# Performance work log

Hardware: AMD Instinct MI355X
Metric: run time of the kernel (lower is better)

The kernel has to match this reference:

```python
import jax, jax.numpy as jnp
import numpy as np

N = 8192   # decoder nodes (batch*seq)
M = 8192   # encoder memory nodes
D = 512    # d_model (layer.size)
H = 8      # attention heads
DK = D // H
DFF = 2048 # feed-forward hidden
E = 262144 # edges per attention graph (avg in-degree 32)
EPS = 1e-6


def _ln(x, g, b):
    # LayerNorm over last dim (annotated-transformer style, eps=1e-6)
    mu = x.mean(-1, keepdims=True)
    var = ((x - mu) ** 2).mean(-1, keepdims=True)
    return (x - mu) * jax.lax.rsqrt(var + EPS) * g + b


def _heads(t):
    return t.reshape(-1, H, DK)


def _attend(q, k, v, src, dst, n_dst):
    # per-edge score = exp(clip(k_src . q_dst / sqrt(dk))), scatter-sum to dst
    score = jnp.einsum('ehd,ehd->eh', k[src], q[dst]) * np.float32(1.0 / np.sqrt(DK))
    score = jnp.exp(jnp.clip(score, -10.0, 10.0))
    wv = jax.ops.segment_sum(score[:, :, None] * v[src], dst, num_segments=n_dst)  # [n_dst,H,DK]
    z = jax.ops.segment_sum(score, dst, num_segments=n_dst)                         # [n_dst,H]
    return (wv / z[:, :, None]).reshape(n_dst, D)


def setup_inputs() -> dict:
    key = jax.random.key(0)
    ks = jax.random.split(key, 16)
    f = lambda k, shape, s: jax.random.normal(k, shape, dtype=jnp.float32) * np.float32(s)
    inp = {
        'x': f(ks[0], (N, D), 1.0),
        'mem': f(ks[1], (M, D), 1.0),
        'ln0_g': jnp.ones((D,), jnp.float32), 'ln0_b': jnp.zeros((D,), jnp.float32),
        'ln1_g': jnp.ones((D,), jnp.float32), 'ln1_b': jnp.zeros((D,), jnp.float32),
        'ln2_g': jnp.ones((D,), jnp.float32), 'ln2_b': jnp.zeros((D,), jnp.float32),
        'Wq': f(ks[2], (D, D), D ** -0.5), 'bq': jnp.zeros((D,), jnp.float32),
        'Wk': f(ks[3], (D, D), D ** -0.5), 'bk': jnp.zeros((D,), jnp.float32),
        'Wv': f(ks[4], (D, D), D ** -0.5), 'bv': jnp.zeros((D,), jnp.float32),
        'Wo': f(ks[5], (D, D), D ** -0.5), 'bo': jnp.zeros((D,), jnp.float32),
        'W1': f(ks[6], (D, DFF), D ** -0.5), 'b1': jnp.zeros((DFF,), jnp.float32),
        'W2': f(ks[7], (DFF, D), DFF ** -0.5), 'b2': jnp.zeros((D,), jnp.float32),
        'src_self': jax.random.randint(ks[8], (E,), 0, N),
        'dst_self': jax.random.randint(ks[9], (E,), 0, N),
        'src_cross': jax.random.randint(ks[10], (E,), 0, M),
        'dst_cross': jax.random.randint(ks[11], (E,), 0, N),
    }
    return inp


def reference(x, mem, ln0_g, ln0_b, ln1_g, ln1_b, ln2_g, ln2_b,
              Wq, bq, Wk, bk, Wv, bv, Wo, bo, W1, b1, W2, b2,
              src_self, dst_self, src_cross, dst_cross):
    # l=0: self-attention. pre_func('qkv',0): norm then qkv projections.
    h = _ln(x, ln0_g, ln0_b)
    q = _heads(h @ Wq + bq)
    k = _heads(h @ Wk + bk)
    v = _heads(h @ Wv + bv)
    # post_func(0): o = W_o(wv/z); x = x + dropout(o) (eval: identity)
    o = _attend(q, k, v, src_self, dst_self, N) @ Wo + bo
    x = x + o
    # l=1: cross-attention. pre_func('q',1): norm on decoder nodes;
    # pre_func('kv'): NO norm on memory nodes (norm_x = x branch).
    h = _ln(x, ln1_g, ln1_b)
    q = _heads(h @ Wq + bq)
    km = _heads(mem @ Wk + bk)
    vm = _heads(mem @ Wv + bv)
    o = _attend(q, km, vm, src_cross, dst_cross, N) @ Wo + bo
    x = x + o
    # post_func(1): feed-forward sublayer x + dropout(FF(LN(x)))
    h = _ln(x, ln2_g, ln2_b)
    x = x + (jax.nn.relu(h @ W1 + b1) @ W2 + b2)
    return x
```

## Files before the change

### kernel.cpp

```cpp
#include <hip/hip_runtime.h>
#include <cstdint>
#include <cstddef>

#define DEV __device__ __forceinline__

typedef __attribute__((ext_vector_type(4))) float f32x4;
typedef __attribute__((ext_vector_type(2))) float f32x2;
typedef __attribute__((ext_vector_type(4))) unsigned int u32x4;
typedef __attribute__((ext_vector_type(2))) unsigned int u32x2;
typedef unsigned short ushort_t;

constexpr int NN  = 8192;
constexpr int MMM = 8192;
constexpr int DD  = 512;
constexpr int DFF = 2048;

DEV unsigned short f2bf(float f) {
  unsigned int u = __builtin_bit_cast(unsigned int, f);
  u += 0x7fffu + ((u >> 16) & 1u);
  return (unsigned short)(u >> 16);
}
DEV float bflo(unsigned int u) { return __builtin_bit_cast(float, u << 16); }
DEV float bfhi(unsigned int u) { return __builtin_bit_cast(float, u & 0xffff0000u); }
DEV unsigned char f2fp8(float f) {
  int p = __builtin_amdgcn_cvt_pk_fp8_f32(f, f, 0, false);
  return (unsigned char)(p & 0xff);
}

DEV void gload_lds16(const void* g, void* l) {
  __builtin_amdgcn_global_load_lds((__attribute__((address_space(1))) void*)g,
                                   (__attribute__((address_space(3))) void*)l,
                                   16, 0, 0);
}

__global__ void transw_kernel(const float* __restrict__ in, ushort_t* __restrict__ out,
                              int R, int C) {
  __shared__ float t[32][33];
  const int x0 = blockIdx.x * 32, y0 = blockIdx.y * 32;
  const int tx = threadIdx.x, ty = threadIdx.y;
#pragma unroll
  for (int i = 0; i < 4; ++i)
    t[ty + i * 8][tx] = in[(long)(y0 + ty + i * 8) * C + x0 + tx];
  __syncthreads();
#pragma unroll
  for (int i = 0; i < 4; ++i)
    out[(long)(x0 + ty + i * 8) * R + y0 + tx] = f2bf(t[tx][ty + i * 8]);
}

struct TW4 {
  const float* in0; const float* in1; const float* in2; const float* in3;
  ushort_t* o0; ushort_t* o1; ushort_t* o2; ushort_t* o3;
};
__global__ void transw4_kernel(TW4 p) {
  const float* in; ushort_t* out;
  switch (blockIdx.z) {
    case 0:  in = p.in0; out = p.o0; break;
    case 1:  in = p.in1; out = p.o1; break;
    case 2:  in = p.in2; out = p.o2; break;
    default: in = p.in3; out = p.o3; break;
  }
  __shared__ float t[32][33];
  const int x0 = blockIdx.x * 32, y0 = blockIdx.y * 32;
  const int tx = threadIdx.x, ty = threadIdx.y;
#pragma unroll
  for (int i = 0; i < 4; ++i)
    t[ty + i * 8][tx] = in[(long)(y0 + ty + i * 8) * 512 + x0 + tx];
  __syncthreads();
#pragma unroll
  for (int i = 0; i < 4; ++i)
    out[(long)(x0 + ty + i * 8) * 512 + y0 + tx] = f2bf(t[tx][ty + i * 8]);
}

__global__ void tobf_kernel(const float* __restrict__ in, ushort_t* __restrict__ out, int n4) {
  int i = blockIdx.x * blockDim.x + threadIdx.x;
  if (i >= n4) return;
  f32x4 v = ((const f32x4*)in)[i];
  u32x2 o;
  o[0] = (unsigned)f2bf(v[0]) | ((unsigned)f2bf(v[1]) << 16);
  o[1] = (unsigned)f2bf(v[2]) | ((unsigned)f2bf(v[3]) << 16);
  ((u32x2*)out)[i] = o;
}

__global__ void biascat_kernel(const float* __restrict__ bq, const float* __restrict__ bk,
                               const float* __restrict__ bv, float* __restrict__ o) {
  const int i = blockIdx.x * blockDim.x + threadIdx.x;
  if (i >= 1536) return;
  o[i] = (i < 512) ? bq[i] : ((i < 1024) ? bk[i - 512] : bv[i - 1024]);
}

__global__ __launch_bounds__(256)
void ln_kernel(const float* __restrict__ x, const float* __restrict__ g,
               const float* __restrict__ b, ushort_t* __restrict__ out) {
  const int row  = blockIdx.x * 4 + (threadIdx.x >> 6);
  const int lane = threadIdx.x & 63;
  const float* xr = x + (long)row * DD + lane * 8;
  float v[8];
  *(f32x4*)&v[0] = *(const f32x4*)&xr[0];
  *(f32x4*)&v[4] = *(const f32x4*)&xr[4];
  float s = 0.f, sq = 0.f;
#pragma unroll
  for (int i = 0; i < 8; ++i) { s += v[i]; sq += v[i] * v[i]; }
#pragma unroll
  for (int o = 1; o < 64; o <<= 1) { s += __shfl_xor(s, o); sq += __shfl_xor(sq, o); }
  const float mu   = s * (1.f / 512.f);
  const float var  = sq * (1.f / 512.f) - mu * mu;
  const float rstd = rsqrtf(var + 1e-6f);
  const float* gp = g + lane * 8;
  const float* bp = b + lane * 8;
  u32x4 o8;
#pragma unroll
  for (int u = 0; u < 4; ++u) {
    unsigned int lo = f2bf((v[2 * u]     - mu) * rstd * gp[2 * u]     + bp[2 * u]);
    unsigned int hi = f2bf((v[2 * u + 1] - mu) * rstd * gp[2 * u + 1] + bp[2 * u + 1]);
    o8[u] = lo | (hi << 16);
  }
  *(u32x4*)(out + (long)row * DD + lane * 8) = o8;
}


template <int EPI>
__global__ __launch_bounds__(256, 2)
void gemm_kernel(const ushort_t* __restrict__ A, const ushort_t* __restrict__ Bt,
                 const float* __restrict__ bias, const float* res,
                 float* outF, ushort_t* outB, unsigned char* out8, int M, int N, int K) {
  __shared__ __align__(16) ushort_t sA[128 * 64];
  __shared__ __align__(16) ushort_t sB[128 * 64];
  const int tid  = threadIdx.x;
  const int lane = tid & 63;
  const int w    = tid >> 6;
  const int wr   = w >> 1, wc = w & 1;
  const long brow = (long)blockIdx.x * 128;
  const long bcol = (long)blockIdx.y * 128;
  const int r16 = lane & 15;
  const int cq  = lane >> 4;
  f32x4 acc[4][4] = {};

  for (int k0 = 0; k0 < K; k0 += 64) {
    __syncthreads();
#pragma unroll
    for (int i = 0; i < 4; ++i) {
      const int c   = i * 256 + tid;
      const int wb  = i * 256 + (tid & ~63);
      const int row = c >> 3;
      const int col = ((c & 7) ^ (row & 7)) << 3;
      gload_lds16(A  + (brow + row) * (long)K + k0 + col, &sA[(long)wb * 8]);
      gload_lds16(Bt + (bcol + row) * (long)K + k0 + col, &sB[(long)wb * 8]);
    }
    __syncthreads();
#pragma unroll
    for (int kkc = 0; kkc < 8; kkc += 4) {
      u32x4 af[4], bfr[4];
#pragma unroll
      for (int i = 0; i < 4; ++i) {
        const int row = wr * 64 + i * 16 + r16;
        af[i] = *(const u32x4*)&sA[row * 64 + (((kkc + cq) ^ (row & 7)) << 3)];
      }
#pragma unroll
      for (int j = 0; j < 4; ++j) {
        const int row = wc * 64 + j * 16 + r16;
        bfr[j] = *(const u32x4*)&sB[row * 64 + (((kkc + cq) ^ (row & 7)) << 3)];
      }
#pragma unroll
      for (int i = 0; i < 4; ++i)
#pragma unroll
        for (int j = 0; j < 4; ++j)
          asm("v_mfma_f32_16x16x32_bf16 %0, %1, %2, %0"
              : "+v"(acc[i][j]) : "v"(af[i]), "v"(bfr[j]));
    }
  }
  asm volatile("s_nop 7\n\ts_nop 7\n\ts_nop 7" ::);

  const long orow = brow + wr * 64;
  const long ocol = bcol + wc * 64;
#pragma unroll
  for (int j = 0; j < 4; ++j) {
    const long c  = ocol + j * 16 + r16;
    const float bv = bias[c];
#pragma unroll
    for (int i = 0; i < 4; ++i) {
      const long r0 = orow + i * 16 + ((lane >> 4) << 2);
#pragma unroll
      for (int r = 0; r < 4; ++r) {
        float v = acc[i][j][r] + bv;
        const long row = r0 + r;
        if (EPI == 0)      outB[row * (long)N + c] = f2bf(v);
        else if (EPI == 1) outB[row * (long)N + c] = f2bf(fmaxf(v, 0.f));
        else if (EPI == 2) outF[row * (long)N + c] = v + res[row * (long)N + c];
        else if (EPI == 3) out8[row * (long)N + c] = f2fp8(v);
        else {
          if (c < 512) outB[row * 512 + c] = f2bf(v);
          else         out8[row * 1024 + (c - 512)] = f2fp8(v);
        }
      }
    }
  }
}

template <int EPI>
__global__ __launch_bounds__(256, 4)
void gemm64b_kernel(const ushort_t* __restrict__ A, const ushort_t* __restrict__ Bt,
                    const float* __restrict__ bias, const float* res,
                    float* outF, ushort_t* outB, unsigned char* out8, int M, int N, int K) {
  __shared__ __align__(16) ushort_t sA[64 * 64];
  __shared__ __align__(16) ushort_t sB[64 * 64];
  const int tid  = threadIdx.x;
  const int lane = tid & 63;
  const int w    = tid >> 6;
  const int wr   = w >> 1, wc = w & 1;
  const long brow = (long)blockIdx.x * 64;
  const long bcol = (long)blockIdx.y * 64;
  const int r16 = lane & 15;
  const int cq  = lane >> 4;
  f32x4 acc[2][2] = {};

  for (int k0 = 0; k0 < K; k0 += 64) {
    __syncthreads();
#pragma unroll
    for (int i = 0; i < 2; ++i) {
      const int c   = i * 256 + tid;
      const int wb  = i * 256 + (tid & ~63);
      const int row = c >> 3;
      const int col = ((c & 7) ^ (row & 7)) << 3;
      gload_lds16(A  + (brow + row) * (long)K + k0 + col, &sA[(long)wb * 8]);
      gload_lds16(Bt + (bcol + row) * (long)K + k0 + col, &sB[(long)wb * 8]);
    }
    __syncthreads();
#pragma unroll
    for (int kkc = 0; kkc < 8; kkc += 4) {
      u32x4 af[2], bfr[2];
#pragma unroll
      for (int i = 0; i < 2; ++i) {
        const int row = wr * 32 + i * 16 + r16;
        af[i] = *(const u32x4*)&sA[row * 64 + (((kkc + cq) ^ (row & 7)) << 3)];
      }
#pragma unroll
      for (int j = 0; j < 2; ++j) {
        const int row = wc * 32 + j * 16 + r16;
        bfr[j] = *(const u32x4*)&sB[row * 64 + (((kkc + cq) ^ (row & 7)) << 3)];
      }
#pragma unroll
      for (int i = 0; i < 2; ++i)
#pragma unroll
        for (int j = 0; j < 2; ++j)
          asm("v_mfma_f32_16x16x32_bf16 %0, %1, %2, %0"
              : "+v"(acc[i][j]) : "v"(af[i]), "v"(bfr[j]));
    }
  }
  asm volatile("s_nop 7\n\ts_nop 7\n\ts_nop 7" ::);

  const long orow = brow + wr * 32;
  const long ocol = bcol + wc * 32;
#pragma unroll
  for (int j = 0; j < 2; ++j) {
    const long c  = ocol + j * 16 + r16;
    const float bv = bias[c];
#pragma unroll
    for (int i = 0; i < 2; ++i) {
      const long r0 = orow + i * 16 + ((lane >> 4) << 2);
#pragma unroll
      for (int r = 0; r < 4; ++r) {
        float v = acc[i][j][r] + bv;
        const long row = r0 + r;
        if (EPI == 0)      outB[row * (long)N + c] = f2bf(v);
        else if (EPI == 1) outB[row * (long)N + c] = f2bf(fmaxf(v, 0.f));
        else if (EPI == 2) outF[row * (long)N + c] = v + res[row * (long)N + c];
        else               out8[row * (long)N + c] = f2fp8(v);
      }
    }
  }
}

__global__ void zero_kernel(int* p, int n) {
  int i = blockIdx.x * blockDim.x + threadIdx.x;
  if (i < n) p[i] = 0;
}
__global__ void hist2_kernel(const int* __restrict__ d0, const int* __restrict__ d1,
                             int* __restrict__ counts2, int E) {
  const int* d = blockIdx.y ? d1 : d0;
  int* c = counts2 + blockIdx.y * 8192;
  for (int e = blockIdx.x * blockDim.x + threadIdx.x; e < E; e += gridDim.x * blockDim.x)
    atomicAdd(&c[d[e]], 1);
}
template <int PER, int BINS>
__global__ void scan_kernel(const int* __restrict__ countsN, int* __restrict__ rowstartN,
                            int* __restrict__ cursorN) {
  const int* counts = countsN + blockIdx.x * BINS;
  int* rowstart = rowstartN + blockIdx.x * (BINS + 1);
  int* cursor   = cursorN + blockIdx.x * BINS;
  __shared__ int part[256];
  const int t = threadIdx.x;
  int loc[PER];
  int s = 0;
  const int base = t * PER;
#pragma unroll
  for (int i = 0; i < PER; ++i) { loc[i] = counts[base + i]; s += loc[i]; }
  part[t] = s;
  __syncthreads();
  for (int off = 1; off < 256; off <<= 1) {
    int v2 = (t >= off) ? part[t - off] : 0;
    __syncthreads();
    part[t] += v2;
    __syncthreads();
  }
  int run = part[t] - s;
#pragma unroll
  for (int i = 0; i < PER; ++i) { rowstart[base + i] = run; cursor[base + i] = run; run += loc[i]; }
  if (t == 255) rowstart[BINS] = run;
}
__global__ void scatterS_kernel(const int* __restrict__ s0, const int* __restrict__ d0,
                                const int* __restrict__ s1, const int* __restrict__ d1,
                                int* __restrict__ cursor2, int* __restrict__ countsD2,
                                int2* __restrict__ oSD0, int2* __restrict__ oSD1, int E) {
  const int* s = blockIdx.y ? s1 : s0;
  const int* d = blockIdx.y ? d1 : d0;
  int* cur  = cursor2 + blockIdx.y * 8192;
  int* cntD = countsD2 + blockIdx.y * 8192;
  int2* o = blockIdx.y ? oSD1 : oSD0;
  for (int e = blockIdx.x * blockDim.x + threadIdx.x; e < E; e += gridDim.x * blockDim.x) {
    const int sv = s[e];
    const int dv = d[e];
    const int p = atomicAdd(&cur[sv], 1);
    o[p] = make_int2(sv, dv);
    atomicAdd(&cntD[dv], 1);
  }
}
__global__ void scatterD_kernel(const int2* __restrict__ sd0, const int2* __restrict__ sd1,
                                int* __restrict__ cursorD2,
                                int* __restrict__ o0, int* __restrict__ o1, int E) {
  const int2* sd = blockIdx.y ? sd1 : sd0;
  int* cur = cursorD2 + blockIdx.y * 8192;
  int* o = blockIdx.y ? o1 : o0;
  for (int e = blockIdx.x * blockDim.x + threadIdx.x; e < E; e += gridDim.x * blockDim.x) {
    const int2 t = sd[e];
    const int p = atomicAdd(&cur[t.y], 1);
    o[p] = t.x;
  }
}

#define ATT_LOADI(SD, EB)                                                   \
  _Pragma("unroll") for (int jj = 0; jj < 4; ++jj) {                        \
    int e_ = (EB) + jj;                                                     \
    SD[jj] = srcs[e_ < e1 ? e_ : e1 - 1];                                   \
  }
#define ATT_LOADG(KD, VD, SD)                                               \
  _Pragma("unroll") for (int jj = 0; jj < 4; ++jj) {                        \
    const unsigned char* p_ = kvb + (long)SD[jj] * 1024 + boff;             \
    KD[jj] = *(const u32x2*)p_;                                             \
    VD[jj] = *(const u32x2*)(p_ + 512);                                     \
  }
#define ATT_EDGE(KF, VF, VALID)                                             \
  {                                                                         \
    f32x2 d2_ = {0.f, 0.f};                                                 \
    d2_ += (f32x2)__builtin_amdgcn_cvt_pk_f32_fp8((KF)[0], false) * q2[0];  \
    d2_ += (f32x2)__builtin_amdgcn_cvt_pk_f32_fp8((KF)[0], true)  * q2[1];  \
    d2_ += (f32x2)__builtin_amdgcn_cvt_pk_f32_fp8((KF)[1], false) * q2[2];  \
    d2_ += (f32x2)__builtin_amdgcn_cvt_pk_f32_fp8((KF)[1], true)  * q2[3];  \
    float dot_ = d2_[0] + d2_[1];                                           \
    dot_ += __shfl_xor(dot_, 1);                                            \
    dot_ += __shfl_xor(dot_, 2);                                            \
    dot_ += __shfl_xor(dot_, 4);                                            \
    float sc_ = __expf(fminf(fmaxf(dot_ * 0.125f, -10.f), 10.f));           \
    sc_ = (VALID) ? sc_ : 0.f;                                              \
    z += sc_;                                                               \
    const f32x2 s2_ = {sc_, sc_};                                           \
    av[0] += s2_ * (f32x2)__builtin_amdgcn_cvt_pk_f32_fp8((VF)[0], false);  \
    av[1] += s2_ * (f32x2)__builtin_amdgcn_cvt_pk_f32_fp8((VF)[0], true);   \
    av[2] += s2_ * (f32x2)__builtin_amdgcn_cvt_pk_f32_fp8((VF)[1], false);  \
    av[3] += s2_ * (f32x2)__builtin_amdgcn_cvt_pk_f32_fp8((VF)[1], true);   \
  }
#define ATT_GROUP(GB, K4, V4)                                               \
  _Pragma("unroll") for (int jj = 0; jj < 4; ++jj) {                        \
    ATT_EDGE(K4[jj], V4[jj], ((GB) + jj < n))                               \
  }

__global__ __launch_bounds__(256)
void attend_kernel(const int* __restrict__ rowstart, const int* __restrict__ srcs,
                   const ushort_t* __restrict__ qb,
                   const unsigned char* __restrict__ kvb,
                   ushort_t* __restrict__ ob) {
  const int d    = blockIdx.x * 4 + (threadIdx.x >> 6);
  const int lane = threadIdx.x & 63;
  const int boff = lane * 8;
  const int e0 = rowstart[d], e1 = rowstart[d + 1];
  const int n  = e1 - e0;
  const u32x4 qv = *(const u32x4*)(qb + (long)d * DD + lane * 8);
  f32x2 q2[4];
#pragma unroll
  for (int u = 0; u < 4; ++u) q2[u] = f32x2{bflo(qv[u]), bfhi(qv[u])};
  f32x2 av[4] = {};
  float z = 0.f;
  if (n > 0) {
    int sA4[4], sB4[4];
    u32x2 kA4[4], vA4[4], kB4[4], vB4[4];
    ATT_LOADI(sA4, e0);
    ATT_LOADI(sB4, e0 + 4);
    ATT_LOADG(kA4, vA4, sA4);
    const int ng = (n + 3) >> 2;
    const int NG = (ng + 1) & ~1;
    for (int g = 0; g < NG; g += 2) {
      ATT_LOADG(kB4, vB4, sB4);
      ATT_LOADI(sA4, e0 + (g + 2) * 4);
      ATT_GROUP(g * 4, kA4, vA4)
      ATT_LOADG(kA4, vA4, sA4);
      ATT_LOADI(sB4, e0 + (g + 3) * 4);
      ATT_GROUP((g + 1) * 4, kB4, vB4)
    }
  }
  const float inv = 1.f / z;
  u32x4 o;
#pragma unroll
  for (int u = 0; u < 4; ++u)
    o[u] = (unsigned)f2bf(av[u][0] * inv) | ((unsigned)f2bf(av[u][1] * inv) << 16);
  *(u32x4*)(ob + (long)d * DD + lane * 8) = o;
}

extern "C" void kernel_launch(void* const* d_in, const int* in_sizes, int n_in,
                              void* d_out, int out_size, void* d_ws, size_t ws_size,
                              hipStream_t stream) {
  const float* x    = (const float*)d_in[0];
  const float* mem  = (const float*)d_in[1];
  const float* ln0g = (const float*)d_in[2];  const float* ln0b = (const float*)d_in[3];
  const float* ln1g = (const float*)d_in[4];  const float* ln1b = (const float*)d_in[5];
  const float* ln2g = (const float*)d_in[6];  const float* ln2b = (const float*)d_in[7];
  const float* Wq = (const float*)d_in[8];   const float* bq = (const float*)d_in[9];
  const float* Wk = (const float*)d_in[10];  const float* bk = (const float*)d_in[11];
  const float* Wv = (const float*)d_in[12];  const float* bv = (const float*)d_in[13];
  const float* Wo = (const float*)d_in[14];  const float* bo = (const float*)d_in[15];
  const float* W1 = (const float*)d_in[16];  const float* b1 = (const float*)d_in[17];
  const float* W2 = (const float*)d_in[18];  const float* b2 = (const float*)d_in[19];
  const int* src_self  = (const int*)d_in[20];
  const int* dst_self  = (const int*)d_in[21];
  const int* src_cross = (const int*)d_in[22];
  const int* dst_cross = (const int*)d_in[23];
  const int E = in_sizes[20];
  float* out = (float*)d_out;

  char* wsp = (char*)d_ws;
  auto alloc = [&](size_t bytes) {
    char* p = wsp;
    wsp += (bytes + 255) & ~(size_t)255;
    return p;
  };
  ushort_t* Wqkv_t = (ushort_t*)alloc((size_t)1536 * 512 * 2);
  ushort_t* Wo_t   = (ushort_t*)alloc((size_t)512 * 512 * 2);
  ushort_t* W1_t   = (ushort_t*)alloc((size_t)DFF * DD * 2);
  ushort_t* W2_t   = (ushort_t*)alloc((size_t)DD * DFF * 2);
  float*    bqkv   = (float*)alloc(1536 * 4);
  ushort_t* h_bf   = (ushort_t*)alloc((size_t)NN * DD * 2);
  ushort_t* mem_bf = (ushort_t*)alloc((size_t)MMM * DD * 2);
  ushort_t* q_bf   = (ushort_t*)alloc((size_t)NN * DD * 2);
  unsigned char* kvf8 = (unsigned char*)alloc((size_t)NN * 1024);
  ushort_t* attn_bf= (ushort_t*)alloc((size_t)NN * DD * 2);
  ushort_t* ffh_bf = (ushort_t*)alloc((size_t)NN * DFF * 2);
  int* countsS   = (int*)alloc(2 * 8192 * 4);
  int* countsD   = (int*)alloc(2 * 8192 * 4);
  int* rsS2      = (int*)alloc(2 * 8193 * 4);
  int* curS2     = (int*)alloc(2 * 8192 * 4);
  int* rowstartD2= (int*)alloc(2 * 8193 * 4);
  int* cursorD2  = (int*)alloc(2 * 8192 * 4);
  int2* sdT0     = (int2*)alloc((size_t)E * 8);
  int2* sdT1     = (int2*)alloc((size_t)E * 8);
  int* srcsA     = (int*)alloc((size_t)E * 4);
  int* srcsB     = (int*)alloc((size_t)E * 4);

  const dim3 B256(256);

  TW4 tw{Wq, Wk, Wv, Wo, Wqkv_t, Wqkv_t + 512 * 512, Wqkv_t + 1024 * 512, Wo_t};
  transw4_kernel<<<dim3(16, 16, 4), dim3(32, 8), 0, stream>>>(tw);
  transw_kernel<<<dim3(64, 16), dim3(32, 8), 0, stream>>>(W1, W1_t, DD, DFF);
  transw_kernel<<<dim3(16, 64), dim3(32, 8), 0, stream>>>(W2, W2_t, DFF, DD);
  biascat_kernel<<<dim3(6), B256, 0, stream>>>(bq, bk, bv, bqkv);
  tobf_kernel<<<dim3(MMM * DD / 4 / 256), B256, 0, stream>>>(mem, mem_bf, MMM * DD / 4);
  zero_kernel<<<dim3(128), B256, 0, stream>>>(countsS, 4 * 8192);
  hist2_kernel<<<dim3(256, 2), B256, 0, stream>>>(src_self, src_cross, countsS, E);
  scan_kernel<32, 8192><<<dim3(2), B256, 0, stream>>>(countsS, rsS2, curS2);
  scatterS_kernel<<<dim3(256, 2), B256, 0, stream>>>(src_self, dst_self, src_cross, dst_cross,
                                                     curS2, countsD, sdT0, sdT1, E);
  scan_kernel<32, 8192><<<dim3(2), B256, 0, stream>>>(countsD, rowstartD2, cursorD2);
  scatterD_kernel<<<dim3(256, 2), B256, 0, stream>>>(sdT0, sdT1, cursorD2, srcsA, srcsB, E);

  auto gemm = [&](int mode, const ushort_t* Ap, const ushort_t* Btp, const float* biasp,
                  const float* resp, float* oF, ushort_t* oB, unsigned char* o8,
                  int M_, int N_, int K_) {
    if (N_ <= 1024) {
      dim3 g(M_ / 64, N_ / 64);
      if (mode == 0)
        gemm64b_kernel<0><<<g, B256, 0, stream>>>(Ap, Btp, biasp, resp, oF, oB, o8, M_, N_, K_);
      else if (mode == 1)
        gemm64b_kernel<1><<<g, B256, 0, stream>>>(Ap, Btp, biasp, resp, oF, oB, o8, M_, N_, K_);
      else if (mode == 2)
        gemm64b_kernel<2><<<g, B256, 0, stream>>>(Ap, Btp, biasp, resp, oF, oB, o8, M_, N_, K_);
      else
        gemm64b_kernel<3><<<g, B256, 0, stream>>>(Ap, Btp, biasp, resp, oF, oB, o8, M_, N_, K_);
    } else {
      dim3 g(M_ / 128, N_ / 128);
      if (mode == 0)
        gemm_kernel<0><<<g, B256, 0, stream>>>(Ap, Btp, biasp, resp, oF, oB, o8, M_, N_, K_);
      else if (mode == 1)
        gemm_kernel<1><<<g, B256, 0, stream>>>(Ap, Btp, biasp, resp, oF, oB, o8, M_, N_, K_);
      else if (mode == 2)
        gemm_kernel<2><<<g, B256, 0, stream>>>(Ap, Btp, biasp, resp, oF, oB, o8, M_, N_, K_);
      else if (mode == 3)
        gemm_kernel<3><<<g, B256, 0, stream>>>(Ap, Btp, biasp, resp, oF, oB, o8, M_, N_, K_);
      else
        gemm_kernel<4><<<g, B256, 0, stream>>>(Ap, Btp, biasp, resp, oF, oB, o8, M_, N_, K_);
    }
  };

  ln_kernel<<<dim3(NN / 4), B256, 0, stream>>>(x, ln0g, ln0b, h_bf);
  gemm(4, h_bf, Wqkv_t, bqkv, nullptr, nullptr, q_bf, kvf8, NN, 1536, DD);
  attend_kernel<<<dim3(NN / 4), B256, 0, stream>>>(rowstartD2, srcsA, q_bf, kvf8, attn_bf);
  gemm(2, attn_bf, Wo_t, bo, x, out, nullptr, nullptr, NN, DD, DD);

  ln_kernel<<<dim3(NN / 4), B256, 0, stream>>>(out, ln1g, ln1b, h_bf);
  gemm(0, h_bf, Wqkv_t, bqkv, nullptr, nullptr, q_bf, nullptr, NN, 512, DD);
  gemm(3, mem_bf, Wqkv_t + 512 * 512, bqkv + 512, nullptr, nullptr, nullptr, kvf8,
       MMM, 1024, DD);
  attend_kernel<<<dim3(NN / 4), B256, 0, stream>>>(rowstartD2 + 8193, srcsB, q_bf, kvf8, attn_bf);
  gemm(2, attn_bf, Wo_t, bo, out, out, nullptr, nullptr, NN, DD, DD);

  ln_kernel<<<dim3(NN / 4), B256, 0, stream>>>(out, ln2g, ln2b, h_bf);
  gemm(1, h_bf, W1_t, b1, nullptr, nullptr, ffh_bf, nullptr, NN, DFF, DD);
  gemm(2, ffh_bf, W2_t, b2, out, out, nullptr, nullptr, NN, DD, DFF);

  (void)n_in; (void)out_size; (void)ws_size; (void)in_sizes;
}
```

Measured before the change: 334.4 us.

## Build dst-CSR directly and raise GEMM launch-bound occupancy hints

Drops the two-pass counting sort, which first bucketed edges by source and then by destination. Edges now go straight into destination buckets, removing a histogram, a scan, a scatter pass and the intermediate int2 buffers. The source order within each destination bucket is lost, so gathers of K/V rows in the attention kernel may have worse locality. Separately, the launch-bounds minimum-blocks hints on both GEMM kernels are doubled, which may force register limits or spills.

```diff
diff --git a/kernel.cpp b/kernel.cpp
--- a/kernel.cpp
+++ b/kernel.cpp
@@ -119,7 +119,7 @@
 
 
 template <int EPI>
-__global__ __launch_bounds__(256, 2)
+__global__ __launch_bounds__(256, 4)
 void gemm_kernel(const ushort_t* __restrict__ A, const ushort_t* __restrict__ Bt,
                  const float* __restrict__ bias, const float* res,
                  float* outF, ushort_t* outB, unsigned char* out8, int M, int N, int K) {
@@ -197,7 +197,7 @@
 }
 
 template <int EPI>
-__global__ __launch_bounds__(256, 4)
+__global__ __launch_bounds__(256, 8)
 void gemm64b_kernel(const ushort_t* __restrict__ A, const ushort_t* __restrict__ Bt,
                     const float* __restrict__ bias, const float* res,
                     float* outF, ushort_t* outB, unsigned char* out8, int M, int N, int K) {
@@ -307,33 +307,17 @@
   for (int i = 0; i < PER; ++i) { rowstart[base + i] = run; cursor[base + i] = run; run += loc[i]; }
   if (t == 255) rowstart[BINS] = run;
 }
-__global__ void scatterS_kernel(const int* __restrict__ s0, const int* __restrict__ d0,
+__global__ void scatterD_kernel(const int* __restrict__ s0, const int* __restrict__ d0,
                                 const int* __restrict__ s1, const int* __restrict__ d1,
-                                int* __restrict__ cursor2, int* __restrict__ countsD2,
-                                int2* __restrict__ oSD0, int2* __restrict__ oSD1, int E) {
+                                int* __restrict__ cursorD2,
+                                int* __restrict__ o0, int* __restrict__ o1, int E) {
   const int* s = blockIdx.y ? s1 : s0;
   const int* d = blockIdx.y ? d1 : d0;
-  int* cur  = cursor2 + blockIdx.y * 8192;
-  int* cntD = countsD2 + blockIdx.y * 8192;
-  int2* o = blockIdx.y ? oSD1 : oSD0;
-  for (int e = blockIdx.x * blockDim.x + threadIdx.x; e < E; e += gridDim.x * blockDim.x) {
-    const int sv = s[e];
-    const int dv = d[e];
-    const int p = atomicAdd(&cur[sv], 1);
-    o[p] = make_int2(sv, dv);
-    atomicAdd(&cntD[dv], 1);
-  }
-}
-__global__ void scatterD_kernel(const int2* __restrict__ sd0, const int2* __restrict__ sd1,
-                                int* __restrict__ cursorD2,
-                                int* __restrict__ o0, int* __restrict__ o1, int E) {
-  const int2* sd = blockIdx.y ? sd1 : sd0;
   int* cur = cursorD2 + blockIdx.y * 8192;
   int* o = blockIdx.y ? o1 : o0;
   for (int e = blockIdx.x * blockDim.x + threadIdx.x; e < E; e += gridDim.x * blockDim.x) {
-    const int2 t = sd[e];
-    const int p = atomicAdd(&cur[t.y], 1);
-    o[p] = t.x;
+    const int p = atomicAdd(&cur[d[e]], 1);
+    o[p] = s[e];
   }
 }
 
@@ -452,14 +436,9 @@
   unsigned char* kvf8 = (unsigned char*)alloc((size_t)NN * 1024);
   ushort_t* attn_bf= (ushort_t*)alloc((size_t)NN * DD * 2);
   ushort_t* ffh_bf = (ushort_t*)alloc((size_t)NN * DFF * 2);
-  int* countsS   = (int*)alloc(2 * 8192 * 4);
   int* countsD   = (int*)alloc(2 * 8192 * 4);
-  int* rsS2      = (int*)alloc(2 * 8193 * 4);
-  int* curS2     = (int*)alloc(2 * 8192 * 4);
   int* rowstartD2= (int*)alloc(2 * 8193 * 4);
   int* cursorD2  = (int*)alloc(2 * 8192 * 4);
-  int2* sdT0     = (int2*)alloc((size_t)E * 8);
-  int2* sdT1     = (int2*)alloc((size_t)E * 8);
   int* srcsA     = (int*)alloc((size_t)E * 4);
   int* srcsB     = (int*)alloc((size_t)E * 4);
 
@@ -471,13 +450,11 @@
   transw_kernel<<<dim3(16, 64), dim3(32, 8), 0, stream>>>(W2, W2_t, DFF, DD);
   biascat_kernel<<<dim3(6), B256, 0, stream>>>(bq, bk, bv, bqkv);
   tobf_kernel<<<dim3(MMM * DD / 4 / 256), B256, 0, stream>>>(mem, mem_bf, MMM * DD / 4);
-  zero_kernel<<<dim3(128), B256, 0, stream>>>(countsS, 4 * 8192);
-  hist2_kernel<<<dim3(256, 2), B256, 0, stream>>>(src_self, src_cross, countsS, E);
-  scan_kernel<32, 8192><<<dim3(2), B256, 0, stream>>>(countsS, rsS2, curS2);
-  scatterS_kernel<<<dim3(256, 2), B256, 0, stream>>>(src_self, dst_self, src_cross, dst_cross,
-                                                     curS2, countsD, sdT0, sdT1, E);
+  zero_kernel<<<dim3(64), B256, 0, stream>>>(countsD, 2 * 8192);
+  hist2_kernel<<<dim3(256, 2), B256, 0, stream>>>(dst_self, dst_cross, countsD, E);
   scan_kernel<32, 8192><<<dim3(2), B256, 0, stream>>>(countsD, rowstartD2, cursorD2);
-  scatterD_kernel<<<dim3(256, 2), B256, 0, stream>>>(sdT0, sdT1, cursorD2, srcsA, srcsB, E);
+  scatterD_kernel<<<dim3(256, 2), B256, 0, stream>>>(src_self, dst_self, src_cross, dst_cross,
+                                                     cursorD2, srcsA, srcsB, E);
 
   auto gemm = [&](int mode, const ushort_t* Ap, const ushort_t* Btp, const float* biasp,
                   const float* resp, float* oF, ushort_t* oB, unsigned char* o8,
```

New measurement: 286.3 us. 14.4% less time.
